# Optimization experiments

Hardware: AMD Instinct MI355X
Metric: run time of the kernel (lower is better)

The kernel has to match this reference:

```python
import jax, jax.numpy as jnp
import numpy as np

DEPTH = 24
D_MODEL = 384
D_INNER = 768          # expand=2.0
D_STATE = 16
DT_RANK = 24           # ceil(384/16)
D_CONV = 3
PATCH = 16
IMG = 224
N_PATCH = (IMG // PATCH) ** 2  # 196
BATCH = 4


def setup_inputs() -> dict:
    key = jax.random.key(0)
    ks = jax.random.split(key, 12)
    f = lambda k, shape, s=0.02: (jax.random.normal(k, shape) * s).astype(jnp.float32)
    # S4D-real init for A_log, as in mamba
    A_log = jnp.log(jnp.tile(jnp.arange(1, D_STATE + 1, dtype=jnp.float32), (DEPTH, D_INNER, 1)))
    dt_bias = jnp.full((DEPTH, D_INNER), float(np.log(np.expm1(0.01))), dtype=jnp.float32)
    return {
        "z": jax.random.normal(ks[0], (BATCH, 3, IMG, IMG), jnp.float32),
        "x": jax.random.normal(ks[1], (BATCH, 3, IMG, IMG), jnp.float32),
        "patch_W": f(ks[2], (D_MODEL, 3, PATCH, PATCH)),
        "patch_b": jnp.zeros((D_MODEL,), jnp.float32),
        "pos_embed": f(ks[3], (1, N_PATCH + 1, D_MODEL)),
        "norm_w": jnp.ones((DEPTH, D_MODEL), jnp.float32),
        "norm_b": jnp.zeros((DEPTH, D_MODEL), jnp.float32),
        "in_W": f(ks[4], (DEPTH, 2 * D_INNER, D_MODEL)),
        "conv_W": f(ks[5], (DEPTH, D_INNER, D_CONV), 0.2),
        "conv_b": jnp.zeros((DEPTH, D_INNER), jnp.float32),
        "xproj_W": f(ks[6], (DEPTH, DT_RANK + 2 * D_STATE, D_INNER)),
        "dtproj_W": f(ks[7], (DEPTH, D_INNER, DT_RANK), 0.1),
        "dtproj_b": dt_bias,
        "A_log": A_log,
        "D_param": jnp.ones((DEPTH, D_INNER), jnp.float32),
        "out_W": f(ks[8], (DEPTH, D_MODEL, D_INNER)),
        "fnorm_w": jnp.ones((D_MODEL,), jnp.float32),
        "fnorm_b": jnp.zeros((D_MODEL,), jnp.float32),
    }


def _layernorm(x, w, b):
    mu = jnp.mean(x, axis=-1, keepdims=True)
    var = jnp.var(x, axis=-1, keepdims=True)
    return (x - mu) * jax.lax.rsqrt(var + 1e-5) * w + b


def _mixer(x, iw, cw, cb, xw, dw, db, al, dd, ow):
    # x: (B, L, d_model)
    B_, L, _ = x.shape
    xz = jnp.einsum('bld,ed->ble', x, iw)            # (B, L, 2*d_inner)
    xs, zg = jnp.split(xz, 2, axis=-1)
    # depthwise causal conv1d along L (kernel D_CONV)
    xp = jnp.pad(xs, ((0, 0), (D_CONV - 1, 0), (0, 0)))
    xc = cb + sum(xp[:, j:j + L, :] * cw[:, j] for j in range(D_CONV))
    xc = jax.nn.silu(xc)
    dbl = jnp.einsum('bld,ed->ble', xc, xw)          # (B, L, dt_rank + 2*N)
    dt = dbl[..., :DT_RANK]
    Bm = dbl[..., DT_RANK:DT_RANK + D_STATE]         # (B, L, N)
    Cm = dbl[..., DT_RANK + D_STATE:]                # (B, L, N)
    dt = jax.nn.softplus(jnp.einsum('blr,dr->bld', dt, dw) + db)  # (B, L, d_inner)
    A = -jnp.exp(al)                                  # (d_inner, N)
    dA = jnp.exp(dt[..., None] * A)                   # (B, L, d_inner, N)
    dBu = (dt * xc)[..., None] * Bm[:, :, None, :]    # (B, L, d_inner, N)

    def step(h, inp):
        dA_t, dBu_t, C_t = inp
        h = dA_t * h + dBu_t
        return h, jnp.einsum('bdn,bn->bd', h, C_t)

    h0 = jnp.zeros((B_, D_INNER, D_STATE), x.dtype)
    _, ys = jax.lax.scan(step, h0, (dA.transpose(1, 0, 2, 3), dBu.transpose(1, 0, 2, 3), Cm.transpose(1, 0, 2)))
    y = ys.transpose(1, 0, 2) + dd * xc               # (B, L, d_inner)
    y = y * jax.nn.silu(zg)
    return jnp.einsum('ble,de->bld', y, ow)           # (B, L, d_model)


def reference(z, x, patch_W, patch_b, pos_embed, norm_w, norm_b, in_W, conv_W, conv_b,
              xproj_W, dtproj_W, dtproj_b, A_log, D_param, out_W, fnorm_w, fnorm_b):
    def embed(img):
        feat = jax.lax.conv_general_dilated(img, patch_W, (PATCH, PATCH), 'VALID',
                                            dimension_numbers=('NCHW', 'OIHW', 'NCHW'))
        B_, C, H, W = feat.shape
        feat = feat.reshape(B_, C, H * W).transpose(0, 2, 1) + patch_b  # (B, 196, d)
        return feat + pos_embed[:, 1:, :]

    h = jnp.concatenate([embed(z), embed(x)], axis=1)  # (B, 392, d)

    def block(carry, p):
        nw, nb, iw, cw, cb, xw, dw, db, al, dd, ow = p
        y = _layernorm(carry, nw, nb)
        y = _mixer(y, iw, cw, cb, xw, dw, db, al, dd, ow)
        return carry + y, None

    h, _ = jax.lax.scan(block, h, (norm_w, norm_b, in_W, conv_W, conv_b, xproj_W,
                                   dtproj_W, dtproj_b, A_log, D_param, out_W))
    return _layernorm(h, fnorm_w, fnorm_b)
```

## Files before the change

kernel.cpp:

```cpp
#include <hip/hip_runtime.h>

typedef unsigned short u16;
typedef unsigned int   u32;

#define B_     4
#define L_     392
#define T_     1568
#define DM     384
#define DI     768
#define DS     16
#define DTR    24
#define DEPTH_ 24
#define NPATCH 196
#define NC     28
#define CL     14

#define XKC    96
#define XPAD   104
#define OKC    384
#define OPAD   392

typedef __bf16 bf16x8 __attribute__((ext_vector_type(8)));
typedef float  f32x4  __attribute__((ext_vector_type(4)));
typedef u16    u16x4  __attribute__((ext_vector_type(4)));

__device__ __forceinline__ u16 f2bf(float f) {
  union { float f; u32 u; } v; v.f = f;
  return (u16)((v.u + 0x7fffu + ((v.u >> 16) & 1u)) >> 16);
}
__device__ __forceinline__ float bf2f(u16 h) {
  union { u32 u; float f; } v; v.u = (u32)h << 16; return v.f;
}

__global__ __launch_bounds__(256) void cvt3v_kernel(const float* __restrict__ s0, u16* __restrict__ o0, int m0,
                                                    const float* __restrict__ s1, u16* __restrict__ o1, int m1,
                                                    const float* __restrict__ s2, u16* __restrict__ o2, int m2) {
  int i = blockIdx.x * 256 + threadIdx.x;
  const float* s; u16* o;
  if (i < m0)      { s = s0; o = o0; }
  else { i -= m0;
  if (i < m1)      { s = s1; o = o1; }
  else { i -= m1;
  if (i < m2)      { s = s2; o = o2; }
  else return; } }
  float4 v = ((const float4*)s)[i];
  u16x4 r;
  r.x = f2bf(v.x); r.y = f2bf(v.y); r.z = f2bf(v.z); r.w = f2bf(v.w);
  ((u16x4*)o)[i] = r;
}

__global__ __launch_bounds__(256) void repack_inW_kernel(const float* __restrict__ src,
                                                         u16* __restrict__ dst) {
  int idx = blockIdx.x * 256 + threadIdx.x;
  const int total = DEPTH_ * 2 * DI * DM / 4;
  if (idx >= total) return;
  float4 v = ((const float4*)src)[idx];
  int k4   = idx % (DM / 4);
  int rest = idx / (DM / 4);
  int row  = rest % (2 * DI);
  int ly   = rest / (2 * DI);
  int k = k4 * 4;
  size_t o = (size_t)ly * (2 * DI * DM)
           + ((size_t)(row >> 4) * 48 + (k >> 3)) * 128
           + (size_t)(row & 15) * 8 + (k & 7);
  u16x4 r;
  r.x = f2bf(v.x); r.y = f2bf(v.y); r.z = f2bf(v.z); r.w = f2bf(v.w);
  *(u16x4*)(dst + o) = r;
}

__global__ __launch_bounds__(256) void imcol_kernel(const float* __restrict__ z,
                                                    const float* __restrict__ x,
                                                    u16* __restrict__ out) {
  int idx = blockIdx.x * 256 + threadIdx.x;
  int t = idx / 768, k = idx - t * 768;
  int b = t / L_, l = t - b * L_;
  const float* img = (l < NPATCH) ? z : x;
  int p  = (l < NPATCH) ? l : l - NPATCH;
  int py = p / 14, px = p - py * 14;
  int ic = k >> 8, rem = k & 255, i = rem >> 4, j = rem & 15;
  float v = img[((size_t)b * 3 + ic) * 50176 + (size_t)(py * 16 + i) * 224 + (px * 16 + j)];
  out[idx] = f2bf(v);
}

__global__ __launch_bounds__(256) void gemm_bf16(const u16* __restrict__ A,
                                                 const u16* __restrict__ W,
                                                 float* __restrict__ outf,
                                                 int M, int N, int K) {
  int wave = threadIdx.x >> 6;
  int lane = threadIdx.x & 63;
  int r = lane & 15, quad = lane >> 4;
  int m_base = blockIdx.x * 64;
  int n_base = blockIdx.y * 64 + wave * 16;

  const u16* aptr[4];
#pragma unroll
  for (int mi = 0; mi < 4; ++mi) {
    int row = m_base + mi * 16 + r; if (row > M - 1) row = M - 1;
    aptr[mi] = A + (size_t)row * K + quad * 8;
  }
  int wcol = n_base + r; if (wcol > N - 1) wcol = N - 1;
  const u16* wptr = W + (size_t)wcol * K + quad * 8;

  f32x4 acc[4] = {f32x4{0,0,0,0}, f32x4{0,0,0,0}, f32x4{0,0,0,0}, f32x4{0,0,0,0}};
  for (int k0 = 0; k0 < K; k0 += 32) {
    bf16x8 bfrag = *(const bf16x8*)(wptr + k0);
#pragma unroll
    for (int mi = 0; mi < 4; ++mi) {
      bf16x8 afrag = *(const bf16x8*)(aptr[mi] + k0);
      acc[mi] = __builtin_amdgcn_mfma_f32_16x16x32_bf16(afrag, bfrag, acc[mi], 0, 0, 0);
    }
  }
  int ccol = n_base + r;
  if (ccol < N) {
#pragma unroll
    for (int mi = 0; mi < 4; ++mi) {
#pragma unroll
      for (int rr = 0; rr < 4; ++rr) {
        int crow = m_base + mi * 16 + quad * 4 + rr;
        if (crow < M) outf[(size_t)crow * N + ccol] = acc[mi][rr];
      }
    }
  }
}

__global__ __launch_bounds__(256) void gemm_ln(const float* __restrict__ h,
                                               const float* __restrict__ lw,
                                               const float* __restrict__ lb,
                                               const u16* __restrict__ W3,
                                               u16* __restrict__ xzt) {
  __shared__ u16 atile[64][392];
  int tid = threadIdx.x;
  int w = tid >> 6, l = tid & 63;
  int tok0 = blockIdx.y * 64;

  const int cA = 4 * l;
  const int cB = 256 + 4 * l;
  float4 wA = *(const float4*)(lw + cA);
  float4 bA = *(const float4*)(lb + cA);
  float4 wB = make_float4(0.f, 0.f, 0.f, 0.f), bB = wB;
  if (l < 32) { wB = *(const float4*)(lw + cB); bB = *(const float4*)(lb + cB); }

#pragma unroll 4
  for (int tt = 0; tt < 16; ++tt) {
    int t = w * 16 + tt;
    int tg = tok0 + t; if (tg > T_ - 1) tg = T_ - 1;
    const float* hrow = h + (size_t)tg * DM;
    float4 a = *(const float4*)(hrow + cA);
    float4 b2 = make_float4(0.f, 0.f, 0.f, 0.f);
    if (l < 32) b2 = *(const float4*)(hrow + cB);
    float s  = a.x + a.y + a.z + a.w + b2.x + b2.y + b2.z + b2.w;
    float s2 = a.x * a.x + a.y * a.y + a.z * a.z + a.w * a.w
             + b2.x * b2.x + b2.y * b2.y + b2.z * b2.z + b2.w * b2.w;
#pragma unroll
    for (int o = 32; o; o >>= 1) { s += __shfl_xor(s, o); s2 += __shfl_xor(s2, o); }
    float mu = s * (1.f / DM);
    float rs = rsqrtf(s2 * (1.f / DM) - mu * mu + 1e-5f);
    u16x4 r4;
    r4.x = f2bf((a.x - mu) * rs * wA.x + bA.x);
    r4.y = f2bf((a.y - mu) * rs * wA.y + bA.y);
    r4.z = f2bf((a.z - mu) * rs * wA.z + bA.z);
    r4.w = f2bf((a.w - mu) * rs * wA.w + bA.w);
    *(u16x4*)&atile[t][cA] = r4;
    if (l < 32) {
      u16x4 r4b;
      r4b.x = f2bf((b2.x - mu) * rs * wB.x + bB.x);
      r4b.y = f2bf((b2.y - mu) * rs * wB.y + bB.y);
      r4b.z = f2bf((b2.z - mu) * rs * wB.z + bB.z);
      r4b.w = f2bf((b2.w - mu) * rs * wB.w + bB.w);
      *(u16x4*)&atile[t][cB] = r4b;
    }
  }
  __syncthreads();

  int r = l & 15, u = l >> 4;
  int pbase = blockIdx.x * 4;
  const u16* wp = W3 + ((size_t)pbase * 48 + (size_t)u) * 128 + (size_t)r * 8;
  const u16* lp = &atile[w * 16 + r][u * 8];

  f32x4 acc[4] = {f32x4{0,0,0,0}, f32x4{0,0,0,0}, f32x4{0,0,0,0}, f32x4{0,0,0,0}};
#pragma unroll
  for (int k0 = 0; k0 < DM; k0 += 32) {
    bf16x8 bfrag = *(const bf16x8*)(lp + k0);
#pragma unroll
    for (int mi = 0; mi < 4; ++mi) {
      bf16x8 afrag = *(const bf16x8*)(wp + ((size_t)mi * 48 + (k0 >> 3)) * 128);
      acc[mi] = __builtin_amdgcn_mfma_f32_16x16x32_bf16(afrag, bfrag, acc[mi], 0, 0, 0);
    }
  }
  int ccol = tok0 + w * 16 + r;
  if (ccol < T_) {
#pragma unroll
    for (int mi = 0; mi < 4; ++mi) {
#pragma unroll
      for (int rr2 = 0; rr2 < 4; ++rr2) {
        int crow = pbase * 16 + mi * 16 + u * 4 + rr2;
        xzt[(size_t)crow * T_ + ccol] = f2bf(acc[mi][rr2]);
      }
    }
  }
}

__global__ __launch_bounds__(256) void xproj_conv(const u16* __restrict__ xzt,
                                                  const float* __restrict__ cw,
                                                  const float* __restrict__ cb,
                                                  const u16* __restrict__ Wx,
                                                  float* __restrict__ dbl) {
  __shared__ u16 tile[64][XPAD];
  int t0 = blockIdx.x * 64;
  int kbeg = blockIdx.z * XKC;
  int tid = threadIdx.x;
  int tl = tid & 63, rq = tid >> 6;
  int t = t0 + tl;
  int tc = (t < T_) ? t : T_ - 1;
  int l = tc % L_;
  for (int kkb = rq * 2; kkb < XKC; kkb += 8) {
    u32 pack = 0;
#pragma unroll
    for (int ss = 0; ss < 2; ++ss) {
      int d = kbeg + kkb + ss;
      const u16* row = xzt + (size_t)d * T_ + tc;
      float acc = cb[d] + cw[d * 3 + 2] * bf2f(row[0]);
      if (l >= 1) acc += cw[d * 3 + 1] * bf2f(row[-1]);
      if (l >= 2) acc += cw[d * 3 + 0] * bf2f(row[-2]);
      float v = acc / (1.f + __expf(-acc));
      pack |= (u32)f2bf(v) << (16 * ss);
    }
    *(u32*)&tile[tl][kkb] = pack;
  }
  __syncthreads();

  int wave = tid >> 6, lane = tid & 63;
  int r = lane & 15, quad = lane >> 4;
  int wcol = wave * 16 + r; int wc = (wcol < 56) ? wcol : 55;
  const u16* wptr = Wx + (size_t)wc * DI + kbeg + quad * 8;

  f32x4 acc4[4] = {f32x4{0,0,0,0}, f32x4{0,0,0,0}, f32x4{0,0,0,0}, f32x4{0,0,0,0}};
#pragma unroll
  for (int k0 = 0; k0 < XKC; k0 += 32) {
    bf16x8 bfrag = *(const bf16x8*)(wptr + k0);
#pragma unroll
    for (int mi = 0; mi < 4; ++mi) {
      bf16x8 afrag = *(const bf16x8*)&tile[mi * 16 + r][k0 + quad * 8];
      acc4[mi] = __builtin_amdgcn_mfma_f32_16x16x32_bf16(afrag, bfrag, acc4[mi], 0, 0, 0);
    }
  }
  if (wcol < 56) {
#pragma unroll
    for (int mi = 0; mi < 4; ++mi) {
#pragma unroll
      for (int rr = 0; rr < 4; ++rr) {
        int crow = t0 + mi * 16 + quad * 4 + rr;
        if (crow < T_) atomicAdd(&dbl[(size_t)crow * 56 + wcol], acc4[mi][rr]);
      }
    }
  }
}

__global__ __launch_bounds__(256) void gemm_out(const u16* __restrict__ yt,
                                                const u16* __restrict__ Wo,
                                                float* __restrict__ h) {
  __shared__ u16 tile[64][OPAD];
  int t0 = blockIdx.x * 64;
  int n0 = blockIdx.y * 64;
  int kbeg = blockIdx.z * OKC;
  int tid = threadIdx.x;
  {
    int tl2 = tid & 31, rq = tid >> 5;
    for (int kk = rq; kk < OKC; kk += 8) {
      int d = kbeg + kk;
      u32 v = *(const u32*)(yt + (size_t)d * T_ + t0 + tl2 * 2);
      tile[tl2 * 2][kk]     = (u16)v;
      tile[tl2 * 2 + 1][kk] = (u16)(v >> 16);
    }
  }
  __syncthreads();

  int wave = tid >> 6, lane = tid & 63;
  int r = lane & 15, quad = lane >> 4;
  const u16* wptr = Wo + (size_t)(n0 + wave * 16 + r) * DI + kbeg + quad * 8;

  f32x4 acc[4] = {f32x4{0,0,0,0}, f32x4{0,0,0,0}, f32x4{0,0,0,0}, f32x4{0,0,0,0}};
#pragma unroll
  for (int k0 = 0; k0 < OKC; k0 += 32) {
    bf16x8 bfrag = *(const bf16x8*)(wptr + k0);
#pragma unroll
    for (int mi = 0; mi < 4; ++mi) {
      bf16x8 afrag = *(const bf16x8*)&tile[mi * 16 + r][k0 + quad * 8];
      acc[mi] = __builtin_amdgcn_mfma_f32_16x16x32_bf16(afrag, bfrag, acc[mi], 0, 0, 0);
    }
  }
  int ccol = n0 + wave * 16 + r;
#pragma unroll
  for (int mi = 0; mi < 4; ++mi) {
#pragma unroll
    for (int rr = 0; rr < 4; ++rr) {
      int crow = t0 + mi * 16 + quad * 4 + rr;
      if (crow < T_) atomicAdd(&h[(size_t)crow * DM + ccol], acc[mi][rr]);
    }
  }
}

__global__ __launch_bounds__(256) void biaspos_kernel(float* __restrict__ h,
                                                      const float* __restrict__ pb,
                                                      const float* __restrict__ pos,
                                                      float* __restrict__ dblz) {
  int idx = blockIdx.x * 256 + threadIdx.x;
  if (idx < 2 * T_ * 56) dblz[idx] = 0.f;
  int t = idx / DM, c = idx - t * DM;
  int p = (t % L_) % NPATCH;
  h[idx] += pb[c] + pos[(size_t)(1 + p) * DM + c];
}

__global__ __launch_bounds__(384) void ln_kernel(const float* __restrict__ x,
                                                 const float* __restrict__ w,
                                                 const float* __restrict__ b,
                                                 float* __restrict__ out_f) {
  int t = blockIdx.x;
  int i = threadIdx.x;
  float v = x[(size_t)t * DM + i];
  float s = v, s2 = v * v;
#pragma unroll
  for (int o = 32; o; o >>= 1) { s += __shfl_xor(s, o); s2 += __shfl_xor(s2, o); }
  __shared__ float ls[6], ls2[6];
  int wv = i >> 6;
  if ((i & 63) == 0) { ls[wv] = s; ls2[wv] = s2; }
  __syncthreads();
  float ts = 0.f, ts2 = 0.f;
#pragma unroll
  for (int j = 0; j < 6; ++j) { ts += ls[j]; ts2 += ls2[j]; }
  float mu  = ts * (1.f / DM);
  float var = ts2 * (1.f / DM) - mu * mu;
  float rs  = rsqrtf(var + 1e-5f);
  out_f[(size_t)t * DM + i] = (v - mu) * rs * w[i] + b[i];
}

__global__ __launch_bounds__(448) void scan_kernel(const u16* __restrict__ xzt,
                                                   const float* __restrict__ dbl,
                                                   const float* __restrict__ cw,
                                                   const float* __restrict__ cb,
                                                   const float* __restrict__ dtW,
                                                   const float* __restrict__ dtB,
                                                   const float* __restrict__ Alog,
                                                   const float* __restrict__ Dp,
                                                   u16* __restrict__ yt,
                                                   float* __restrict__ dblz) {
  int bd = blockIdx.x;
  int d  = bd % DI;
  int b  = bd / DI;
  int tid = threadIdx.x;
  int n = tid & 15, c = tid >> 4;

  __shared__ float dtsh[L_];
  __shared__ float zsh[L_];
  __shared__ float xcsh[L_];
  __shared__ float Psh[NC][DS], Ssh[NC][DS], Hsh[NC][DS];
  __shared__ float hC[L_][17];

  {
    int i0 = blockIdx.x * 29 + tid;
    if (tid < 29 && i0 < T_ * 56) dblz[i0] = 0.f;
  }

  const float* wr = dtW + (size_t)d * DTR;
  float bias = dtB[d];
  float w0 = cw[d * 3 + 0], w1 = cw[d * 3 + 1], w2 = cw[d * 3 + 2], cbd = cb[d];
  const u16* xrow = xzt + (size_t)d * T_ + b * L_;
  const u16* zrow = xzt + (size_t)(DI + d) * T_ + b * L_;
  if (tid < L_) {
    int l = tid;
    const float* dr = dbl + (size_t)(b * L_ + l) * 56;
    float s = bias;
#pragma unroll
    for (int j = 0; j < DTR; ++j) s += dr[j] * wr[j];
    dtsh[l] = (s > 20.f) ? s : log1pf(__expf(s));
    float zv = bf2f(zrow[l]);
    zsh[l] = zv / (1.f + __expf(-zv));
    float a = cbd + w2 * bf2f(xrow[l]);
    if (l >= 1) a += w1 * bf2f(xrow[l - 1]);
    if (l >= 2) a += w0 * bf2f(xrow[l - 2]);
    xcsh[l] = a / (1.f + __expf(-a));
  }
  float A  = -__expf(Alog[(size_t)d * DS + n]);
  float Dd = Dp[d];
  __syncthreads();

  int tb = b * L_ + c * CL;
  const float* Bp = dbl + (size_t)tb * 56 + DTR + n;
  const float* Cp = Bp + DS;

  float dA[CL], dBu[CL];
  {
    float P = 1.f, S = 0.f;
#pragma unroll
    for (int l = 0; l < CL; ++l) {
      float dtv = dtsh[c * CL + l];
      float xcv = xcsh[c * CL + l];
      float Bv  = Bp[l * 56];
      float e = __expf(dtv * A);
      float u = dtv * xcv * Bv;
      dA[l] = e; dBu[l] = u;
      P *= e;
      S = e * S + u;
    }
    Psh[c][n] = P; Ssh[c][n] = S;
  }
  __syncthreads();
  if (tid < DS) {
    float hh = 0.f;
#pragma unroll
    for (int cc = 0; cc < NC; ++cc) {
      Hsh[cc][tid] = hh;
      hh = Psh[cc][tid] * hh + Ssh[cc][tid];
    }
  }
  __syncthreads();
  {
    float hh = Hsh[c][n];
#pragma unroll
    for (int l = 0; l < CL; ++l) {
      hh = dA[l] * hh + dBu[l];
      hC[c * CL + l][n] = hh * Cp[l * 56];
    }
  }
  __syncthreads();
  if (tid < L_) {
    int l = tid;
    float p = 0.f;
#pragma unroll
    for (int k = 0; k < DS; ++k) p += hC[l][k];
    yt[(size_t)d * T_ + b * L_ + l] = f2bf((p + Dd * xcsh[l]) * zsh[l]);
  }
}

extern "C" void kernel_launch(void* const* d_in, const int* in_sizes, int n_in,
                              void* d_out, int out_size, void* d_ws, size_t ws_size,
                              hipStream_t stream) {
  const float* z      = (const float*)d_in[0];
  const float* x      = (const float*)d_in[1];
  const float* patchW = (const float*)d_in[2];
  const float* patchB = (const float*)d_in[3];
  const float* pos    = (const float*)d_in[4];
  const float* normW  = (const float*)d_in[5];
  const float* normB  = (const float*)d_in[6];
  const float* inW    = (const float*)d_in[7];
  const float* convW  = (const float*)d_in[8];
  const float* convB  = (const float*)d_in[9];
  const float* xprojW = (const float*)d_in[10];
  const float* dtW    = (const float*)d_in[11];
  const float* dtB    = (const float*)d_in[12];
  const float* Alog   = (const float*)d_in[13];
  const float* Dpar   = (const float*)d_in[14];
  const float* outW   = (const float*)d_in[15];
  const float* fnW    = (const float*)d_in[16];
  const float* fnB    = (const float*)d_in[17];
  float* out = (float*)d_out;

  char* base = (char*)d_ws; size_t off = 0;
  auto alloc = [&](size_t bytes) {
    void* p = base + off; off = (off + bytes + 255) & ~(size_t)255; return p;
  };
  float* h    = (float*)alloc((size_t)T_ * DM * 4);
  u16*   xzt  = (u16*)  alloc((size_t)2 * DI * T_ * 2);
  float* dbl  = (float*)alloc((size_t)2 * T_ * 56 * 4);
  u16*   yt   = (u16*)  alloc((size_t)DI * T_ * 2);
  u16*   imcol= (u16*)  alloc((size_t)T_ * 768 * 2);
  u16*   pwB  = (u16*)  alloc((size_t)DM * 768 * 2);
  u16*   inWb = (u16*)  alloc((size_t)DEPTH_ * 2 * DI * DM * 2);
  u16*   xpWb = (u16*)  alloc((size_t)DEPTH_ * 56 * DI * 2);
  u16*   outWb= (u16*)  alloc((size_t)DEPTH_ * DM * DI * 2);

  {
    int m0 = DM * 768 / 4;
    int m1 = DEPTH_ * 56 * DI / 4;
    int m2 = DEPTH_ * DM * DI / 4;
    int mt = m0 + m1 + m2;
    cvt3v_kernel<<<dim3((mt + 255) / 256), 256, 0, stream>>>(
        patchW, pwB, m0, xprojW, xpWb, m1, outW, outWb, m2);
    int mi4 = DEPTH_ * 2 * DI * DM / 4;
    repack_inW_kernel<<<dim3((mi4 + 255) / 256), 256, 0, stream>>>(inW, inWb);
  }

  imcol_kernel<<<dim3(T_ * 768 / 256), 256, 0, stream>>>(z, x, imcol);
  gemm_bf16<<<dim3((T_ + 63) / 64, DM / 64), 256, 0, stream>>>(
      imcol, pwB, h, T_, DM, 768);
  biaspos_kernel<<<dim3(T_ * DM / 256), 256, 0, stream>>>(h, patchB, pos, dbl);

  const int TG = (T_ + 63) / 64;
  for (int ly = 0; ly < DEPTH_; ++ly) {
    int p = ly & 1;
    float* dblc = dbl + (size_t)p * T_ * 56;
    float* dbln = dbl + (size_t)(p ^ 1) * T_ * 56;
    gemm_ln<<<dim3((2 * DI) / 64, TG), 256, 0, stream>>>(
        h, normW + (size_t)ly * DM, normB + (size_t)ly * DM,
        inWb + (size_t)ly * 2 * DI * DM, xzt);
    xproj_conv<<<dim3(TG, 1, DI / XKC), 256, 0, stream>>>(
        xzt, convW + (size_t)ly * DI * 3, convB + (size_t)ly * DI,
        xpWb + (size_t)ly * 56 * DI, dblc);
    scan_kernel<<<dim3(B_ * DI), 448, 0, stream>>>(
        xzt, dblc, convW + (size_t)ly * DI * 3, convB + (size_t)ly * DI,
        dtW + (size_t)ly * DI * DTR, dtB + (size_t)ly * DI,
        Alog + (size_t)ly * DI * DS, Dpar + (size_t)ly * DI, yt, dbln);
    gemm_out<<<dim3(TG, DM / 64, DI / OKC), 256, 0, stream>>>(
        yt, outWb + (size_t)ly * DM * DI, h);
  }

  ln_kernel<<<dim3(T_), dim3(DM), 0, stream>>>(h, fnW, fnB, out);
}
```

Baseline: 2.087 ms.

## Repack weights into MFMA fragment layout, fuse patch bias, drop out-proj split-K atomics

All weight conversions are merged into one repack kernel that writes patch, x-proj and out-proj weights in the same 16-row fragment-tiled layout already used for in_W, padding x-proj to 64 rows with zeros and also zeroing the dbl buffer. The patch-embedding GEMM reads a fragment-tiled im2col buffer and adds bias and position embedding in its epilogue, which removes the separate bias kernel. gemm_out now loops over both K halves inside one block and does a plain read-modify-write on h instead of atomics. The aim is coalesced fragment loads and fewer launches, in exchange for half as many gemm_out blocks.

```diff
diff --git a/kernel.cpp b/kernel.cpp
--- a/kernel.cpp
+++ b/kernel.cpp
@@ -32,40 +32,65 @@
   union { u32 u; float f; } v; v.u = (u32)h << 16; return v.f;
 }
 
-__global__ __launch_bounds__(256) void cvt3v_kernel(const float* __restrict__ s0, u16* __restrict__ o0, int m0,
-                                                    const float* __restrict__ s1, u16* __restrict__ o1, int m1,
-                                                    const float* __restrict__ s2, u16* __restrict__ o2, int m2) {
+#define RP_M0 73728
+#define RP_M1 3538944
+#define RP_M2 258048
+#define RP_M3 1769472
+#define RP_M4 36864
+#define RP_M5 43904
+#define RP_TOT (RP_M0+RP_M1+RP_M2+RP_M3+RP_M4+RP_M5)
+
+__global__ __launch_bounds__(256) void repack_kernel(
+    const float* __restrict__ patchW, u16* __restrict__ pwB,
+    const float* __restrict__ inW,    u16* __restrict__ inWb,
+    const float* __restrict__ xpW,    u16* __restrict__ xpWb,
+    const float* __restrict__ outW,   u16* __restrict__ outWb,
+    float* __restrict__ dblz) {
   int i = blockIdx.x * 256 + threadIdx.x;
-  const float* s; u16* o;
-  if (i < m0)      { s = s0; o = o0; }
-  else { i -= m0;
-  if (i < m1)      { s = s1; o = o1; }
-  else { i -= m1;
-  if (i < m2)      { s = s2; o = o2; }
-  else return; } }
-  float4 v = ((const float4*)s)[i];
-  u16x4 r;
-  r.x = f2bf(v.x); r.y = f2bf(v.y); r.z = f2bf(v.z); r.w = f2bf(v.w);
-  ((u16x4*)o)[i] = r;
-}
-
-__global__ __launch_bounds__(256) void repack_inW_kernel(const float* __restrict__ src,
-                                                         u16* __restrict__ dst) {
-  int idx = blockIdx.x * 256 + threadIdx.x;
-  const int total = DEPTH_ * 2 * DI * DM / 4;
-  if (idx >= total) return;
-  float4 v = ((const float4*)src)[idx];
-  int k4   = idx % (DM / 4);
-  int rest = idx / (DM / 4);
-  int row  = rest % (2 * DI);
-  int ly   = rest / (2 * DI);
-  int k = k4 * 4;
-  size_t o = (size_t)ly * (2 * DI * DM)
-           + ((size_t)(row >> 4) * 48 + (k >> 3)) * 128
-           + (size_t)(row & 15) * 8 + (k & 7);
-  u16x4 r;
-  r.x = f2bf(v.x); r.y = f2bf(v.y); r.z = f2bf(v.z); r.w = f2bf(v.w);
-  *(u16x4*)(dst + o) = r;
+  const float* src = nullptr; u16* dst = nullptr; size_t o = 0;
+  if (i < RP_M0) {
+    int k = (i % 192) * 4; int row = i / 192;
+    o = ((size_t)(row >> 4) * 96 + (k >> 3)) * 128 + (size_t)(row & 15) * 8 + (k & 7);
+    src = patchW; dst = pwB;
+  } else { i -= RP_M0;
+  if (i < RP_M1) {
+    int k = (i % 96) * 4; int rest = i / 96;
+    int row = rest % 1536, ly = rest / 1536;
+    o = (size_t)ly * 589824 + ((size_t)(row >> 4) * 48 + (k >> 3)) * 128
+      + (size_t)(row & 15) * 8 + (k & 7);
+    src = inW; dst = inWb;
+  } else { i -= RP_M1;
+  if (i < RP_M2) {
+    int k = (i % 192) * 4; int rest = i / 192;
+    int row = rest % 56, ly = rest / 56;
+    o = (size_t)ly * 49152 + ((size_t)(row >> 4) * 96 + (k >> 3)) * 128
+      + (size_t)(row & 15) * 8 + (k & 7);
+    src = xpW; dst = xpWb;
+  } else { i -= RP_M2;
+  if (i < RP_M3) {
+    int k = (i % 192) * 4; int rest = i / 192;
+    int row = rest % 384, ly = rest / 384;
+    o = (size_t)ly * 294912 + ((size_t)(row >> 4) * 96 + (k >> 3)) * 128
+      + (size_t)(row & 15) * 8 + (k & 7);
+    src = outW; dst = outWb;
+  } else { i -= RP_M3;
+  if (i < RP_M4) {
+    int ly = i / 1536, rem = i % 1536;
+    int kb = rem >> 4, rr = (rem >> 1) & 7, half = rem & 1;
+    size_t oz = (size_t)ly * 49152 + (size_t)(288 + kb) * 128 + (size_t)(8 + rr) * 8 + half * 4;
+    u16x4 zz = {0, 0, 0, 0};
+    *(u16x4*)(xpWb + oz) = zz;
+    return;
+  } else { i -= RP_M4;
+  if (i < RP_M5) {
+    ((float4*)dblz)[i] = make_float4(0.f, 0.f, 0.f, 0.f);
+    return;
+  }
+  return; } } } } }
+  float4 v = ((const float4*)src)[i];
+  u16x4 r4;
+  r4.x = f2bf(v.x); r4.y = f2bf(v.y); r4.z = f2bf(v.z); r4.w = f2bf(v.w);
+  *(u16x4*)(dst + o) = r4;
 }
 
 __global__ __launch_bounds__(256) void imcol_kernel(const float* __restrict__ z,
@@ -79,45 +104,42 @@
   int py = p / 14, px = p - py * 14;
   int ic = k >> 8, rem = k & 255, i = rem >> 4, j = rem & 15;
   float v = img[((size_t)b * 3 + ic) * 50176 + (size_t)(py * 16 + i) * 224 + (px * 16 + j)];
-  out[idx] = f2bf(v);
-}
-
-__global__ __launch_bounds__(256) void gemm_bf16(const u16* __restrict__ A,
-                                                 const u16* __restrict__ W,
-                                                 float* __restrict__ outf,
-                                                 int M, int N, int K) {
-  int wave = threadIdx.x >> 6;
-  int lane = threadIdx.x & 63;
+  size_t o = ((size_t)(t >> 4) * 96 + (k >> 3)) * 128 + (size_t)(t & 15) * 8 + (k & 7);
+  out[o] = f2bf(v);
+}
+
+__global__ __launch_bounds__(256) void gemm_patch(const u16* __restrict__ Af,
+                                                  const u16* __restrict__ Wf,
+                                                  const float* __restrict__ pb,
+                                                  const float* __restrict__ pos,
+                                                  float* __restrict__ h) {
+  int wave = threadIdx.x >> 6, lane = threadIdx.x & 63;
   int r = lane & 15, quad = lane >> 4;
-  int m_base = blockIdx.x * 64;
-  int n_base = blockIdx.y * 64 + wave * 16;
-
-  const u16* aptr[4];
+  int t0 = blockIdx.x * 64;
+  int p  = blockIdx.y * 4 + wave;
+  const u16* wp  = Wf + ((size_t)p * 96 + quad) * 128 + (size_t)r * 8;
+  const u16* ap0 = Af + ((size_t)(t0 >> 4) * 96 + quad) * 128 + (size_t)r * 8;
+
+  f32x4 acc[4] = {f32x4{0,0,0,0}, f32x4{0,0,0,0}, f32x4{0,0,0,0}, f32x4{0,0,0,0}};
+#pragma unroll
+  for (int k0 = 0; k0 < 768; k0 += 32) {
+    bf16x8 bfrag = *(const bf16x8*)(wp + (size_t)(k0 >> 3) * 128);
+#pragma unroll
+    for (int mi = 0; mi < 4; ++mi) {
+      bf16x8 afrag = *(const bf16x8*)(ap0 + ((size_t)mi * 96 + (k0 >> 3)) * 128);
+      acc[mi] = __builtin_amdgcn_mfma_f32_16x16x32_bf16(afrag, bfrag, acc[mi], 0, 0, 0);
+    }
+  }
+  int ccol = blockIdx.y * 64 + wave * 16 + r;
+  float pbv = pb[ccol];
 #pragma unroll
   for (int mi = 0; mi < 4; ++mi) {
-    int row = m_base + mi * 16 + r; if (row > M - 1) row = M - 1;
-    aptr[mi] = A + (size_t)row * K + quad * 8;
-  }
-  int wcol = n_base + r; if (wcol > N - 1) wcol = N - 1;
-  const u16* wptr = W + (size_t)wcol * K + quad * 8;
-
-  f32x4 acc[4] = {f32x4{0,0,0,0}, f32x4{0,0,0,0}, f32x4{0,0,0,0}, f32x4{0,0,0,0}};
-  for (int k0 = 0; k0 < K; k0 += 32) {
-    bf16x8 bfrag = *(const bf16x8*)(wptr + k0);
-#pragma unroll
-    for (int mi = 0; mi < 4; ++mi) {
-      bf16x8 afrag = *(const bf16x8*)(aptr[mi] + k0);
-      acc[mi] = __builtin_amdgcn_mfma_f32_16x16x32_bf16(afrag, bfrag, acc[mi], 0, 0, 0);
-    }
-  }
-  int ccol = n_base + r;
-  if (ccol < N) {
-#pragma unroll
-    for (int mi = 0; mi < 4; ++mi) {
-#pragma unroll
-      for (int rr = 0; rr < 4; ++rr) {
-        int crow = m_base + mi * 16 + quad * 4 + rr;
-        if (crow < M) outf[(size_t)crow * N + ccol] = acc[mi][rr];
+#pragma unroll
+    for (int rr = 0; rr < 4; ++rr) {
+      int crow = t0 + mi * 16 + quad * 4 + rr;
+      if (crow < T_) {
+        int pp = (crow % L_) % NPATCH;
+        h[(size_t)crow * DM + ccol] = acc[mi][rr] + pbv + pos[(size_t)(1 + pp) * DM + ccol];
       }
     }
   }
@@ -203,7 +225,7 @@
 __global__ __launch_bounds__(256) void xproj_conv(const u16* __restrict__ xzt,
                                                   const float* __restrict__ cw,
                                                   const float* __restrict__ cb,
-                                                  const u16* __restrict__ Wx,
+                                                  const u16* __restrict__ Wx3,
                                                   float* __restrict__ dbl) {
   __shared__ u16 tile[64][XPAD];
   int t0 = blockIdx.x * 64;
@@ -231,13 +253,13 @@
 
   int wave = tid >> 6, lane = tid & 63;
   int r = lane & 15, quad = lane >> 4;
-  int wcol = wave * 16 + r; int wc = (wcol < 56) ? wcol : 55;
-  const u16* wptr = Wx + (size_t)wc * DI + kbeg + quad * 8;
+  int wcol = wave * 16 + r;
+  const u16* wp = Wx3 + ((size_t)wave * 96 + (kbeg >> 3) + quad) * 128 + (size_t)r * 8;
 
   f32x4 acc4[4] = {f32x4{0,0,0,0}, f32x4{0,0,0,0}, f32x4{0,0,0,0}, f32x4{0,0,0,0}};
 #pragma unroll
   for (int k0 = 0; k0 < XKC; k0 += 32) {
-    bf16x8 bfrag = *(const bf16x8*)(wptr + k0);
+    bf16x8 bfrag = *(const bf16x8*)(wp + (size_t)(k0 >> 3) * 128);
 #pragma unroll
     for (int mi = 0; mi < 4; ++mi) {
       bf16x8 afrag = *(const bf16x8*)&tile[mi * 16 + r][k0 + quad * 8];
@@ -257,58 +279,53 @@
 }
 
 __global__ __launch_bounds__(256) void gemm_out(const u16* __restrict__ yt,
-                                                const u16* __restrict__ Wo,
+                                                const u16* __restrict__ Wo3,
                                                 float* __restrict__ h) {
   __shared__ u16 tile[64][OPAD];
   int t0 = blockIdx.x * 64;
-  int n0 = blockIdx.y * 64;
-  int kbeg = blockIdx.z * OKC;
   int tid = threadIdx.x;
-  {
-    int tl2 = tid & 31, rq = tid >> 5;
-    for (int kk = rq; kk < OKC; kk += 8) {
-      int d = kbeg + kk;
-      u32 v = *(const u32*)(yt + (size_t)d * T_ + t0 + tl2 * 2);
-      tile[tl2 * 2][kk]     = (u16)v;
-      tile[tl2 * 2 + 1][kk] = (u16)(v >> 16);
-    }
-  }
-  __syncthreads();
-
   int wave = tid >> 6, lane = tid & 63;
   int r = lane & 15, quad = lane >> 4;
-  const u16* wptr = Wo + (size_t)(n0 + wave * 16 + r) * DI + kbeg + quad * 8;
+  int p = blockIdx.y * 4 + wave;
 
   f32x4 acc[4] = {f32x4{0,0,0,0}, f32x4{0,0,0,0}, f32x4{0,0,0,0}, f32x4{0,0,0,0}};
 #pragma unroll
-  for (int k0 = 0; k0 < OKC; k0 += 32) {
-    bf16x8 bfrag = *(const bf16x8*)(wptr + k0);
-#pragma unroll
-    for (int mi = 0; mi < 4; ++mi) {
-      bf16x8 afrag = *(const bf16x8*)&tile[mi * 16 + r][k0 + quad * 8];
-      acc[mi] = __builtin_amdgcn_mfma_f32_16x16x32_bf16(afrag, bfrag, acc[mi], 0, 0, 0);
-    }
-  }
-  int ccol = n0 + wave * 16 + r;
+  for (int ks = 0; ks < 2; ++ks) {
+    int kbeg = ks * OKC;
+    if (ks) __syncthreads();
+    {
+      int tl2 = tid & 31, rq = tid >> 5;
+      for (int kk = rq; kk < OKC; kk += 8) {
+        int d = kbeg + kk;
+        u32 v = *(const u32*)(yt + (size_t)d * T_ + t0 + tl2 * 2);
+        tile[tl2 * 2][kk]     = (u16)v;
+        tile[tl2 * 2 + 1][kk] = (u16)(v >> 16);
+      }
+    }
+    __syncthreads();
+    const u16* wp = Wo3 + ((size_t)p * 96 + (kbeg >> 3) + quad) * 128 + (size_t)r * 8;
+#pragma unroll
+    for (int k0 = 0; k0 < OKC; k0 += 32) {
+      bf16x8 bfrag = *(const bf16x8*)(wp + (size_t)(k0 >> 3) * 128);
+#pragma unroll
+      for (int mi = 0; mi < 4; ++mi) {
+        bf16x8 afrag = *(const bf16x8*)&tile[mi * 16 + r][k0 + quad * 8];
+        acc[mi] = __builtin_amdgcn_mfma_f32_16x16x32_bf16(afrag, bfrag, acc[mi], 0, 0, 0);
+      }
+    }
+  }
+  int ccol = blockIdx.y * 64 + wave * 16 + r;
 #pragma unroll
   for (int mi = 0; mi < 4; ++mi) {
 #pragma unroll
     for (int rr = 0; rr < 4; ++rr) {
       int crow = t0 + mi * 16 + quad * 4 + rr;
-      if (crow < T_) atomicAdd(&h[(size_t)crow * DM + ccol], acc[mi][rr]);
-    }
-  }
-}
-
-__global__ __launch_bounds__(256) void biaspos_kernel(float* __restrict__ h,
-                                                      const float* __restrict__ pb,
-                                                      const float* __restrict__ pos,
-                                                      float* __restrict__ dblz) {
-  int idx = blockIdx.x * 256 + threadIdx.x;
-  if (idx < 2 * T_ * 56) dblz[idx] = 0.f;
-  int t = idx / DM, c = idx - t * DM;
-  int p = (t % L_) % NPATCH;
-  h[idx] += pb[c] + pos[(size_t)(1 + p) * DM + c];
+      if (crow < T_) {
+        float* hp = &h[(size_t)crow * DM + ccol];
+        *hp = *hp + acc[mi][rr];
+      }
+    }
+  }
 }
 
 __global__ __launch_bounds__(384) void ln_kernel(const float* __restrict__ x,
@@ -463,27 +480,18 @@
   u16*   xzt  = (u16*)  alloc((size_t)2 * DI * T_ * 2);
   float* dbl  = (float*)alloc((size_t)2 * T_ * 56 * 4);
   u16*   yt   = (u16*)  alloc((size_t)DI * T_ * 2);
-  u16*   imcol= (u16*)  alloc((size_t)T_ * 768 * 2);
+  u16*   imcolF=(u16*)  alloc((size_t)100 * 96 * 128 * 2);
   u16*   pwB  = (u16*)  alloc((size_t)DM * 768 * 2);
   u16*   inWb = (u16*)  alloc((size_t)DEPTH_ * 2 * DI * DM * 2);
-  u16*   xpWb = (u16*)  alloc((size_t)DEPTH_ * 56 * DI * 2);
+  u16*   xpWb = (u16*)  alloc((size_t)DEPTH_ * 64 * DI * 2);
   u16*   outWb= (u16*)  alloc((size_t)DEPTH_ * DM * DI * 2);
 
-  {
-    int m0 = DM * 768 / 4;
-    int m1 = DEPTH_ * 56 * DI / 4;
-    int m2 = DEPTH_ * DM * DI / 4;
-    int mt = m0 + m1 + m2;
-    cvt3v_kernel<<<dim3((mt + 255) / 256), 256, 0, stream>>>(
-        patchW, pwB, m0, xprojW, xpWb, m1, outW, outWb, m2);
-    int mi4 = DEPTH_ * 2 * DI * DM / 4;
-    repack_inW_kernel<<<dim3((mi4 + 255) / 256), 256, 0, stream>>>(inW, inWb);
-  }
-
-  imcol_kernel<<<dim3(T_ * 768 / 256), 256, 0, stream>>>(z, x, imcol);
-  gemm_bf16<<<dim3((T_ + 63) / 64, DM / 64), 256, 0, stream>>>(
-      imcol, pwB, h, T_, DM, 768);
-  biaspos_kernel<<<dim3(T_ * DM / 256), 256, 0, stream>>>(h, patchB, pos, dbl);
+  repack_kernel<<<dim3((RP_TOT + 255) / 256), 256, 0, stream>>>(
+      patchW, pwB, inW, inWb, xprojW, xpWb, outW, outWb, dbl);
+
+  imcol_kernel<<<dim3(T_ * 768 / 256), 256, 0, stream>>>(z, x, imcolF);
+  gemm_patch<<<dim3((T_ + 63) / 64, DM / 64), 256, 0, stream>>>(
+      imcolF, pwB, patchB, pos, h);
 
   const int TG = (T_ + 63) / 64;
   for (int ly = 0; ly < DEPTH_; ++ly) {
@@ -495,12 +503,12 @@
         inWb + (size_t)ly * 2 * DI * DM, xzt);
     xproj_conv<<<dim3(TG, 1, DI / XKC), 256, 0, stream>>>(
         xzt, convW + (size_t)ly * DI * 3, convB + (size_t)ly * DI,
-        xpWb + (size_t)ly * 56 * DI, dblc);
+        xpWb + (size_t)ly * 64 * DI, dblc);
     scan_kernel<<<dim3(B_ * DI), 448, 0, stream>>>(
         xzt, dblc, convW + (size_t)ly * DI * 3, convB + (size_t)ly * DI,
         dtW + (size_t)ly * DI * DTR, dtB + (size_t)ly * DI,
         Alog + (size_t)ly * DI * DS, Dpar + (size_t)ly * DI, yt, dbln);
-    gemm_out<<<dim3(TG, DM / 64, DI / OKC), 256, 0, stream>>>(
+    gemm_out<<<dim3(TG, DM / 64), 256, 0, stream>>>(
         yt, outWb + (size_t)ly * DM * DI, h);
   }
 
```

New measurement: 2.224 ms. 6.6% more time.
